# Performance work log

Measured on AMD Instinct MI355X. Metric: run time of the kernel, lower is better.

The kernel has to match this reference:

```python
import jax, jax.numpy as jnp
import numpy as np

INPUT_SIZE = 512
HIDDEN_SIZE = 1024
SEQ_LEN = 512
BATCH = 64


def _xavier(key, shape):
    fan_out, fan_in = shape
    limit = float(np.sqrt(6.0 / (fan_in + fan_out)))
    return jax.random.uniform(key, shape, jnp.float32, -limit, limit)


def setup_inputs() -> dict:
    key = jax.random.key(0)
    ks = jax.random.split(key, 10)
    return {
        "x_seq": jax.random.normal(ks[0], (SEQ_LEN, BATCH, INPUT_SIZE), jnp.float32),
        "h": jax.random.normal(ks[1], (BATCH, HIDDEN_SIZE), jnp.float32),
        "U_c": _xavier(ks[2], (HIDDEN_SIZE, INPUT_SIZE)),
        "w_c": jax.random.normal(ks[3], (HIDDEN_SIZE,), jnp.float32),
        "b_c": jax.random.normal(ks[4], (HIDDEN_SIZE,), jnp.float32),
        "U_a": _xavier(ks[5], (HIDDEN_SIZE, INPUT_SIZE)),
        "w_a": jax.random.normal(ks[6], (HIDDEN_SIZE,), jnp.float32),
        "b_a": jax.random.normal(ks[7], (HIDDEN_SIZE,), jnp.float32),
        "U_h": _xavier(ks[8], (HIDDEN_SIZE, INPUT_SIZE)),
        "b_h": jax.random.normal(ks[9], (HIDDEN_SIZE,), jnp.float32),
    }


def reference(x_seq, h, U_c, w_c, b_c, U_a, w_a, b_a, U_h, b_h):
    # Precompute all input projections in one big batched GEMM each:
    # (S, B, I) @ (I, H) -> (S, B, H)
    xc = jnp.einsum("sbi,hi->sbh", x_seq, U_c) + b_c
    xa = jnp.einsum("sbi,hi->sbh", x_seq, U_a) + b_a
    xh = jnp.einsum("sbi,hi->sbh", x_seq, U_h) + b_h

    def step(h, proj):
        pc, pa, ph = proj
        c = jax.nn.sigmoid(pc + w_c * h)
        a = 1.0 + jnp.tanh(pa + w_a * h)
        h_new = c * h + (1.0 - c) * jnp.tanh(ph + a * h)
        return h_new, h_new

    hn, y_seq = jax.lax.scan(step, h, (xc, xa, xh))
    return y_seq, hn
```

## Files before the change

kernel.cpp:

```cpp
#include <hip/hip_runtime.h>
#include <hip/hip_bf16.h>
#include <stdint.h>

#define SEQLEN 512
#define NBATCH 64
#define KDIM   512
#define HDIM   1024
#define MTOT   (SEQLEN * NBATCH)
#define NTOT   (3 * HDIM)
#define STRIDE (NBATCH * HDIM)

typedef __attribute__((ext_vector_type(4))) float f32x4;
typedef _Float16 f16x8 __attribute__((ext_vector_type(8)));

__global__ __launch_bounds__(256) void cvt_x(const float* __restrict__ x,
                                             _Float16* __restrict__ xh,
                                             _Float16* __restrict__ xl) {
    int i = blockIdx.x * 256 + threadIdx.x;
    const float4* s = (const float4*)(x + (size_t)i * 8);
    float4 a = s[0], b = s[1];
    float v[8] = {a.x, a.y, a.z, a.w, b.x, b.y, b.z, b.w};
    f16x8 hi, lo;
#pragma unroll
    for (int j = 0; j < 8; ++j) {
        _Float16 h = (_Float16)v[j];
        hi[j] = h;
        lo[j] = (_Float16)(v[j] - (float)h);
    }
    *(f16x8*)(xh + (size_t)i * 8) = hi;
    *(f16x8*)(xl + (size_t)i * 8) = lo;
}

__global__ __launch_bounds__(256) void cvt_u(const float* __restrict__ Uc,
                                             const float* __restrict__ Ua,
                                             const float* __restrict__ Uh,
                                             _Float16* __restrict__ uh,
                                             _Float16* __restrict__ ul) {
    int i = blockIdx.x * 256 + threadIdx.x;
    int n = i >> 6;
    int kb = (i & 63) * 8;
    const float* src = (n < HDIM) ? (Uc + (size_t)n * KDIM)
                     : (n < 2 * HDIM) ? (Ua + (size_t)(n - HDIM) * KDIM)
                     : (Uh + (size_t)(n - 2 * HDIM) * KDIM);
    const float4* s = (const float4*)(src + kb);
    float4 a = s[0], b = s[1];
    float v[8] = {a.x, a.y, a.z, a.w, b.x, b.y, b.z, b.w};
    f16x8 hi, lo;
#pragma unroll
    for (int j = 0; j < 8; ++j) {
        _Float16 h = (_Float16)v[j];
        hi[j] = h;
        lo[j] = (_Float16)(v[j] - (float)h);
    }
    *(f16x8*)(uh + (size_t)n * KDIM + kb) = hi;
    *(f16x8*)(ul + (size_t)n * KDIM + kb) = lo;
}

#define BM 128
#define BN 128
#define BK 32
#define NT_N (NTOT / BN)
#define GRID ((MTOT / BM) * NT_N)

__device__ __forceinline__ void gload16(const _Float16* g, _Float16* l) {
    __builtin_amdgcn_global_load_lds((const __attribute__((address_space(1))) void*)g,
                                     (__attribute__((address_space(3))) void*)l,
                                     16, 0, 0);
}

__global__ __launch_bounds__(256) void gemm_f16x2(const _Float16* __restrict__ Ah,
                                                  const _Float16* __restrict__ Al,
                                                  const _Float16* __restrict__ Bh,
                                                  const _Float16* __restrict__ Bl,
                                                  float* __restrict__ pc,
                                                  float* __restrict__ pa,
                                                  float* __restrict__ ph) {
    __shared__ _Float16 lds[4 * BM * BK];
    _Float16* sAh = lds;
    _Float16* sAl = lds + BM * BK;
    _Float16* sBh = lds + 2 * BM * BK;
    _Float16* sBl = lds + 3 * BM * BK;

    int bid  = (blockIdx.x & 7) * (GRID / 8) + (blockIdx.x >> 3);
    int bm   = bid / NT_N;
    int bn   = bid % NT_N;
    int tid  = threadIdx.x;
    int lane = tid & 63;
    int wave = tid >> 6;
    int wr   = wave >> 1;
    int wc   = wave & 1;

    size_t row_off = (size_t)(tid >> 2) * KDIM
                   + (size_t)((((tid & 3) ^ ((tid >> 3) & 3))) * 8);
    const _Float16* gah0 = Ah + (size_t)bm * BM * KDIM + row_off;
    const _Float16* gal0 = Al + (size_t)bm * BM * KDIM + row_off;
    const _Float16* gbh0 = Bh + (size_t)bn * BN * KDIM + row_off;
    const _Float16* gbl0 = Bl + (size_t)bn * BN * KDIM + row_off;
    const size_t half_panel = (size_t)64 * KDIM;
    _Float16* lah = sAh + tid * 8;
    _Float16* lal = sAl + tid * 8;
    _Float16* lbh = sBh + tid * 8;
    _Float16* lbl = sBl + tid * 8;

    f32x4 acc[4][4];
#pragma unroll
    for (int mi = 0; mi < 4; ++mi)
#pragma unroll
        for (int ni = 0; ni < 4; ++ni)
            acc[mi][ni] = (f32x4){0.f, 0.f, 0.f, 0.f};

    int ro = lane & 15;
    int ko = (((lane >> 4) ^ ((lane >> 1) & 3)) * 8);

    for (int kt = 0; kt < KDIM / BK; ++kt) {
        int g = kt * BK;
        gload16(gah0 + g, lah);
        gload16(gah0 + half_panel + g, lah + 2048);
        gload16(gal0 + g, lal);
        gload16(gal0 + half_panel + g, lal + 2048);
        gload16(gbh0 + g, lbh);
        gload16(gbh0 + half_panel + g, lbh + 2048);
        gload16(gbl0 + g, lbl);
        gload16(gbl0 + half_panel + g, lbl + 2048);
        __syncthreads();

        f16x8 ah[4], al[4], bh[4], bl[4];
#pragma unroll
        for (int mi = 0; mi < 4; ++mi) {
            int r = (wr * 64 + mi * 16 + ro) * BK + ko;
            ah[mi] = *(const f16x8*)(sAh + r);
            al[mi] = *(const f16x8*)(sAl + r);
        }
#pragma unroll
        for (int ni = 0; ni < 4; ++ni) {
            int r = (wc * 64 + ni * 16 + ro) * BK + ko;
            bh[ni] = *(const f16x8*)(sBh + r);
            bl[ni] = *(const f16x8*)(sBl + r);
        }
#pragma unroll
        for (int mi = 0; mi < 4; ++mi)
#pragma unroll
            for (int ni = 0; ni < 4; ++ni) {
                acc[mi][ni] = __builtin_amdgcn_mfma_f32_16x16x32_f16(
                    ah[mi], bl[ni], acc[mi][ni], 0, 0, 0);
                acc[mi][ni] = __builtin_amdgcn_mfma_f32_16x16x32_f16(
                    al[mi], bh[ni], acc[mi][ni], 0, 0, 0);
                acc[mi][ni] = __builtin_amdgcn_mfma_f32_16x16x32_f16(
                    ah[mi], bh[ni], acc[mi][ni], 0, 0, 0);
            }
        __syncthreads();
    }

    int n0 = bn * BN;
    float* outp; int nb;
    if (n0 < HDIM)            { outp = pc; nb = n0; }
    else if (n0 < 2 * HDIM)   { outp = pa; nb = n0 - HDIM; }
    else                      { outp = ph; nb = n0 - 2 * HDIM; }

#pragma unroll
    for (int mi = 0; mi < 4; ++mi)
#pragma unroll
        for (int ni = 0; ni < 4; ++ni) {
            int m = bm * BM + wr * 64 + mi * 16 + (lane >> 4) * 4;
            int n = nb + wc * 64 + ni * 16 + (lane & 15);
#pragma unroll
            for (int r = 0; r < 4; ++r)
                outp[(size_t)(m + r) * HDIM + n] = acc[mi][ni][r];
        }
}

__global__ __launch_bounds__(256) void recur(const float* __restrict__ pc_a,
                                             const float* __restrict__ pa_a,
                                             float* out,
                                             const float* __restrict__ h0,
                                             const float* __restrict__ wc_,
                                             const float* __restrict__ bc_,
                                             const float* __restrict__ wa_,
                                             const float* __restrict__ ba_,
                                             const float* __restrict__ bh_) {
    int idx = blockIdx.x * 256 + threadIdx.x;
    int j = idx & (HDIM - 1);
    float h  = h0[idx];
    float wc = wc_[j], bc = bc_[j];
    float wa = wa_[j], ba = ba_[j];
    float bh = bh_[j];

#define PF 8
    float pc[PF], pa[PF], ph[PF];
#pragma unroll
    for (int u = 0; u < PF; ++u) {
        pc[u] = pc_a[(size_t)u * STRIDE + idx];
        pa[u] = pa_a[(size_t)u * STRIDE + idx];
        ph[u] = out [(size_t)u * STRIDE + idx];
    }

    for (int sb = 0; sb < SEQLEN; sb += PF) {
#pragma unroll
        for (int u = 0; u < PF; ++u) {
            int s = sb + u;
            float vc = pc[u], va = pa[u], vh = ph[u];
            int sp = s + PF; sp = (sp < SEQLEN) ? sp : (SEQLEN - 1);
            pc[u] = pc_a[(size_t)sp * STRIDE + idx];
            pa[u] = pa_a[(size_t)sp * STRIDE + idx];
            ph[u] = out [(size_t)sp * STRIDE + idx];

            float zc = (vc + bc) + wc * h;
            float za = (va + ba) + wa * h;
            float c  = 1.0f / (1.0f + expf(-zc));
            float a  = 1.0f + tanhf(za);
            float ht = tanhf((vh + bh) + a * h);
            h = c * h + (1.0f - c) * ht;
            out[(size_t)s * STRIDE + idx] = h;
        }
    }
    out[(size_t)SEQLEN * STRIDE + idx] = h;
}

extern "C" void kernel_launch(void* const* d_in, const int* in_sizes, int n_in,
                              void* d_out, int out_size, void* d_ws, size_t ws_size,
                              hipStream_t stream) {
    const float* x_seq = (const float*)d_in[0];
    const float* h0    = (const float*)d_in[1];
    const float* U_c   = (const float*)d_in[2];
    const float* w_c   = (const float*)d_in[3];
    const float* b_c   = (const float*)d_in[4];
    const float* U_a   = (const float*)d_in[5];
    const float* w_a   = (const float*)d_in[6];
    const float* b_a   = (const float*)d_in[7];
    const float* U_h   = (const float*)d_in[8];
    const float* b_h   = (const float*)d_in[9];
    float* out = (float*)d_out;

    char* ws = (char*)d_ws;
    const size_t MB = 1024 * 1024;
    float*    ws_pc = (float*)ws;
    float*    ws_pa = (float*)(ws + 128 * MB);
    _Float16* x_hi  = (_Float16*)(ws + 256 * MB);
    _Float16* x_lo  = (_Float16*)(ws + 288 * MB);
    _Float16* u_hi  = (_Float16*)(ws + 320 * MB);
    _Float16* u_lo  = (_Float16*)(ws + 323 * MB);

    cvt_x<<<dim3(MTOT * KDIM / 8 / 256), dim3(256), 0, stream>>>(x_seq, x_hi, x_lo);
    cvt_u<<<dim3(NTOT * KDIM / 8 / 256), dim3(256), 0, stream>>>(U_c, U_a, U_h, u_hi, u_lo);
    gemm_f16x2<<<dim3(GRID), dim3(256), 0, stream>>>(
        x_hi, x_lo, u_hi, u_lo, ws_pc, ws_pa, out);
    recur<<<dim3(STRIDE / 256), dim3(256), 0, stream>>>(ws_pc, ws_pa, out, h0,
                                                        w_c, b_c, w_a, b_a, b_h);
}
```

Measured before the change: 519.7 us.

## Enlarge GEMM tile to 256x256 with double-buffered LDS and interleaved MFMA phases

The split-f16 GEMM moves from 128x128 tiles with 4 waves to 256x256 tiles with 8 waves. LDS is double-buffered so the next K-tile's global-to-LDS loads overlap the current tile's MFMAs. The compute is split into four quadrant phases with interleaved LDS reads, barriers and setprio, and the blockIdx swizzle is dropped. The recurrence prefetch depth doubles to 16, which raises register pressure and LDS use (128KB per block) and may limit occupancy.

```diff
diff --git a/kernel.cpp b/kernel.cpp
--- a/kernel.cpp
+++ b/kernel.cpp
@@ -56,11 +56,12 @@
     *(f16x8*)(ul + (size_t)n * KDIM + kb) = lo;
 }
 
-#define BM 128
-#define BN 128
+#define BM 256
+#define BN 256
 #define BK 32
 #define NT_N (NTOT / BN)
 #define GRID ((MTOT / BM) * NT_N)
+#define KT_N (KDIM / BK)
 
 __device__ __forceinline__ void gload16(const _Float16* g, _Float16* l) {
     __builtin_amdgcn_global_load_lds((const __attribute__((address_space(1))) void*)g,
@@ -68,87 +69,112 @@
                                      16, 0, 0);
 }
 
-__global__ __launch_bounds__(256) void gemm_f16x2(const _Float16* __restrict__ Ah,
-                                                  const _Float16* __restrict__ Al,
-                                                  const _Float16* __restrict__ Bh,
-                                                  const _Float16* __restrict__ Bl,
-                                                  float* __restrict__ pc,
-                                                  float* __restrict__ pa,
-                                                  float* __restrict__ ph) {
-    __shared__ _Float16 lds[4 * BM * BK];
-    _Float16* sAh = lds;
-    _Float16* sAl = lds + BM * BK;
-    _Float16* sBh = lds + 2 * BM * BK;
-    _Float16* sBl = lds + 3 * BM * BK;
-
-    int bid  = (blockIdx.x & 7) * (GRID / 8) + (blockIdx.x >> 3);
+__device__ __forceinline__ f32x4 mfma16(f16x8 a, f16x8 b, f32x4 c) {
+    return __builtin_amdgcn_mfma_f32_16x16x32_f16(a, b, c, 0, 0, 0);
+}
+
+__global__ __launch_bounds__(512, 2) void gemm_f16x2(const _Float16* __restrict__ Ah,
+                                                     const _Float16* __restrict__ Al,
+                                                     const _Float16* __restrict__ Bh,
+                                                     const _Float16* __restrict__ Bl,
+                                                     float* __restrict__ pc,
+                                                     float* __restrict__ pa,
+                                                     float* __restrict__ ph) {
+    __shared__ _Float16 lds[2][4][BM * BK];
+
+    int bid  = blockIdx.x;
     int bm   = bid / NT_N;
     int bn   = bid % NT_N;
     int tid  = threadIdx.x;
     int lane = tid & 63;
     int wave = tid >> 6;
-    int wr   = wave >> 1;
-    int wc   = wave & 1;
+    int wr   = wave >> 2;
+    int wc   = wave & 3;
 
     size_t row_off = (size_t)(tid >> 2) * KDIM
-                   + (size_t)((((tid & 3) ^ ((tid >> 3) & 3))) * 8);
-    const _Float16* gah0 = Ah + (size_t)bm * BM * KDIM + row_off;
-    const _Float16* gal0 = Al + (size_t)bm * BM * KDIM + row_off;
-    const _Float16* gbh0 = Bh + (size_t)bn * BN * KDIM + row_off;
-    const _Float16* gbl0 = Bl + (size_t)bn * BN * KDIM + row_off;
-    const size_t half_panel = (size_t)64 * KDIM;
-    _Float16* lah = sAh + tid * 8;
-    _Float16* lal = sAl + tid * 8;
-    _Float16* lbh = sBh + tid * 8;
-    _Float16* lbl = sBl + tid * 8;
-
-    f32x4 acc[4][4];
-#pragma unroll
-    for (int mi = 0; mi < 4; ++mi)
-#pragma unroll
-        for (int ni = 0; ni < 4; ++ni)
-            acc[mi][ni] = (f32x4){0.f, 0.f, 0.f, 0.f};
+                   + (size_t)(((tid & 3) ^ ((tid >> 3) & 3)) * 8);
+    const _Float16* gAh = Ah + (size_t)bm * BM * KDIM + row_off;
+    const _Float16* gAl = Al + (size_t)bm * BM * KDIM + row_off;
+    const _Float16* gBh = Bh + (size_t)bn * BN * KDIM + row_off;
+    const _Float16* gBl = Bl + (size_t)bn * BN * KDIM + row_off;
+    const size_t HPAN = (size_t)128 * KDIM;
+    int t8 = tid * 8;
+
+#define STAGE(b, kt) do { int _g = (kt) * BK;                                  \
+    gload16(gAh + _g,        &lds[b][0][t8]);                                  \
+    gload16(gAh + HPAN + _g, &lds[b][0][t8 + 4096]);                           \
+    gload16(gAl + _g,        &lds[b][1][t8]);                                  \
+    gload16(gAl + HPAN + _g, &lds[b][1][t8 + 4096]);                           \
+    gload16(gBh + _g,        &lds[b][2][t8]);                                  \
+    gload16(gBh + HPAN + _g, &lds[b][2][t8 + 4096]);                           \
+    gload16(gBl + _g,        &lds[b][3][t8]);                                  \
+    gload16(gBl + HPAN + _g, &lds[b][3][t8 + 4096]); } while (0)
+
+    f32x4 acc[8][4];
+#pragma unroll
+    for (int i = 0; i < 8; ++i)
+#pragma unroll
+        for (int j = 0; j < 4; ++j)
+            acc[i][j] = (f32x4){0.f, 0.f, 0.f, 0.f};
 
     int ro = lane & 15;
-    int ko = (((lane >> 4) ^ ((lane >> 1) & 3)) * 8);
-
-    for (int kt = 0; kt < KDIM / BK; ++kt) {
-        int g = kt * BK;
-        gload16(gah0 + g, lah);
-        gload16(gah0 + half_panel + g, lah + 2048);
-        gload16(gal0 + g, lal);
-        gload16(gal0 + half_panel + g, lal + 2048);
-        gload16(gbh0 + g, lbh);
-        gload16(gbh0 + half_panel + g, lbh + 2048);
-        gload16(gbl0 + g, lbl);
-        gload16(gbl0 + half_panel + g, lbl + 2048);
-        __syncthreads();
-
-        f16x8 ah[4], al[4], bh[4], bl[4];
-#pragma unroll
-        for (int mi = 0; mi < 4; ++mi) {
-            int r = (wr * 64 + mi * 16 + ro) * BK + ko;
-            ah[mi] = *(const f16x8*)(sAh + r);
-            al[mi] = *(const f16x8*)(sAl + r);
-        }
-#pragma unroll
-        for (int ni = 0; ni < 4; ++ni) {
-            int r = (wc * 64 + ni * 16 + ro) * BK + ko;
-            bh[ni] = *(const f16x8*)(sBh + r);
-            bl[ni] = *(const f16x8*)(sBl + r);
-        }
-#pragma unroll
-        for (int mi = 0; mi < 4; ++mi)
-#pragma unroll
-            for (int ni = 0; ni < 4; ++ni) {
-                acc[mi][ni] = __builtin_amdgcn_mfma_f32_16x16x32_f16(
-                    ah[mi], bl[ni], acc[mi][ni], 0, 0, 0);
-                acc[mi][ni] = __builtin_amdgcn_mfma_f32_16x16x32_f16(
-                    al[mi], bh[ni], acc[mi][ni], 0, 0, 0);
-                acc[mi][ni] = __builtin_amdgcn_mfma_f32_16x16x32_f16(
-                    ah[mi], bh[ni], acc[mi][ni], 0, 0, 0);
-            }
-        __syncthreads();
+    int ko = ((lane >> 4) ^ ((lane >> 1) & 3)) * 8;
+
+    f16x8 a_[4][2], b_[2][2];
+
+#define READ_A(mh) _Pragma("unroll")                                           \
+    for (int i = 0; i < 4; ++i) {                                              \
+        int row = wr * 128 + ((mh) * 4 + i) * 16 + ro;                         \
+        a_[i][0] = *(const f16x8*)(&lds[cur][0][row * BK + ko]);               \
+        a_[i][1] = *(const f16x8*)(&lds[cur][1][row * BK + ko]);               \
+    }
+#define READ_B(nh) _Pragma("unroll")                                           \
+    for (int j = 0; j < 2; ++j) {                                              \
+        int row = wc * 64 + ((nh) * 2 + j) * 16 + ro;                          \
+        b_[j][0] = *(const f16x8*)(&lds[cur][2][row * BK + ko]);               \
+        b_[j][1] = *(const f16x8*)(&lds[cur][3][row * BK + ko]);               \
+    }
+#define MFMA_Q(mh, nh) _Pragma("unroll")                                       \
+    for (int i = 0; i < 4; ++i) _Pragma("unroll")                              \
+        for (int j = 0; j < 2; ++j) {                                          \
+            f32x4 c = acc[(mh) * 4 + i][(nh) * 2 + j];                         \
+            c = mfma16(a_[i][0], b_[j][1], c);                                 \
+            c = mfma16(a_[i][1], b_[j][0], c);                                 \
+            c = mfma16(a_[i][0], b_[j][0], c);                                 \
+            acc[(mh) * 4 + i][(nh) * 2 + j] = c;                               \
+        }
+#define LGKM0 do { asm volatile("s_waitcnt lgkmcnt(0)" ::: "memory");          \
+                   __builtin_amdgcn_sched_barrier(0); } while (0)
+
+    STAGE(0, 0);
+
+    for (int kt = 0; kt < KT_N; ++kt) {
+        int cur = kt & 1;
+        if (kt < KT_N - 1) {
+            STAGE(1 - cur, kt + 1);
+            asm volatile("s_waitcnt vmcnt(8)" ::: "memory");
+        } else {
+            asm volatile("s_waitcnt vmcnt(0)" ::: "memory");
+        }
+        __builtin_amdgcn_s_barrier();
+        asm volatile("" ::: "memory");
+
+        READ_A(0); READ_B(0);
+        LGKM0;
+        __builtin_amdgcn_s_setprio(1); MFMA_Q(0, 0); __builtin_amdgcn_s_setprio(0);
+        READ_B(1);
+        __builtin_amdgcn_s_barrier();
+        LGKM0;
+        __builtin_amdgcn_s_setprio(1); MFMA_Q(0, 1); __builtin_amdgcn_s_setprio(0);
+        READ_A(1);
+        __builtin_amdgcn_s_barrier();
+        LGKM0;
+        __builtin_amdgcn_s_setprio(1); MFMA_Q(1, 1); __builtin_amdgcn_s_setprio(0);
+        READ_B(0);
+        __builtin_amdgcn_s_barrier();
+        LGKM0;
+        __builtin_amdgcn_s_setprio(1); MFMA_Q(1, 0); __builtin_amdgcn_s_setprio(0);
+        __builtin_amdgcn_s_barrier();
     }
 
     int n0 = bn * BN;
@@ -158,15 +184,20 @@
     else                      { outp = ph; nb = n0 - 2 * HDIM; }
 
 #pragma unroll
-    for (int mi = 0; mi < 4; ++mi)
-#pragma unroll
-        for (int ni = 0; ni < 4; ++ni) {
-            int m = bm * BM + wr * 64 + mi * 16 + (lane >> 4) * 4;
-            int n = nb + wc * 64 + ni * 16 + (lane & 15);
+    for (int ai = 0; ai < 8; ++ai)
+#pragma unroll
+        for (int bj = 0; bj < 4; ++bj) {
+            int m = bm * BM + wr * 128 + ai * 16 + (lane >> 4) * 4;
+            int n = nb + wc * 64 + bj * 16 + (lane & 15);
 #pragma unroll
             for (int r = 0; r < 4; ++r)
-                outp[(size_t)(m + r) * HDIM + n] = acc[mi][ni][r];
-        }
+                outp[(size_t)(m + r) * HDIM + n] = acc[ai][bj][r];
+        }
+#undef STAGE
+#undef READ_A
+#undef READ_B
+#undef MFMA_Q
+#undef LGKM0
 }
 
 __global__ __launch_bounds__(256) void recur(const float* __restrict__ pc_a,
@@ -185,7 +216,7 @@
     float wa = wa_[j], ba = ba_[j];
     float bh = bh_[j];
 
-#define PF 8
+#define PF 16
     float pc[PF], pa[PF], ph[PF];
 #pragma unroll
     for (int u = 0; u < PF; ++u) {
@@ -242,7 +273,7 @@
 
     cvt_x<<<dim3(MTOT * KDIM / 8 / 256), dim3(256), 0, stream>>>(x_seq, x_hi, x_lo);
     cvt_u<<<dim3(NTOT * KDIM / 8 / 256), dim3(256), 0, stream>>>(U_c, U_a, U_h, u_hi, u_lo);
-    gemm_f16x2<<<dim3(GRID), dim3(256), 0, stream>>>(
+    gemm_f16x2<<<dim3(GRID), dim3(512), 0, stream>>>(
         x_hi, x_lo, u_hi, u_lo, ws_pc, ws_pa, out);
     recur<<<dim3(STRIDE / 256), dim3(256), 0, stream>>>(ws_pc, ws_pa, out, h0,
                                                         w_c, b_c, w_a, b_a, b_h);
```

Result: faster. 482.8 us (-7.1%).
